# Kernel tuning notes

Hardware: AMD Instinct MI355X
Metric: run time of the kernel (lower is better)

## Reference

```python
import jax, jax.numpy as jnp
import numpy as np

E = 2048      # embed_dim
H = 16        # num_heads
HD = E // H // 2   # differential head dim = 64
S = 2048      # seq len
B = 1         # batch
DEPTH = 12
LAMBDA_INIT = 0.8 - 0.6 * float(np.exp(-0.3 * DEPTH))
EPS = 1e-5


def setup_inputs() -> dict:
    key = jax.random.key(0)
    ks = jax.random.split(key, 12)
    n = lambda k, shape, s=1.0: (jax.random.normal(k, shape, dtype=jnp.float32) * s)
    return {
        "query": n(ks[0], (S, B, E)),
        "key": n(ks[1], (S, B, E)),
        "value": n(ks[2], (S, B, E)),
        "rel_pos": 0,
        "attn_mask": jnp.zeros((B, S), dtype=jnp.bool_),
        "Wq": n(ks[3], (E, E), 0.02),
        "Wk": n(ks[4], (E, E), 0.02),
        "Wv": n(ks[5], (E, E), 0.02),
        "Wo": n(ks[6], (E, E), 0.02),
        "lq1": n(ks[7], (HD,), 0.1),
        "lk1": n(ks[8], (HD,), 0.1),
        "lq2": n(ks[9], (HD,), 0.1),
        "lk2": n(ks[10], (HD,), 0.1),
        "subln_g": jnp.ones((2 * HD,), dtype=jnp.float32),
    }


def reference(query, key, value, rel_pos, attn_mask,
              Wq, Wk, Wv, Wo, lq1, lk1, lq2, lk2, subln_g):
    # (S,B,E) -> (B,S,E)
    q = jnp.einsum("sbe,fe->bsf", query, Wq)
    k = jnp.einsum("sbe,fe->bsf", key, Wk)
    v = jnp.einsum("sbe,fe->bsf", value, Wv)

    bsz, tgt_len, _ = q.shape
    scaling = HD ** -0.5

    q = q.reshape(bsz, tgt_len, 2 * H, HD).transpose(0, 2, 1, 3) * scaling  # (B,2H,S,hd)
    k = k.reshape(bsz, tgt_len, 2 * H, HD).transpose(0, 2, 1, 3)            # (B,2H,S,hd)
    v = v.reshape(bsz, tgt_len, H, 2 * HD).transpose(0, 2, 1, 3)            # (B,H,S,2hd)

    scores = jnp.einsum("bhqd,bhkd->bhqk", q, k)  # (B,2H,S,S)
    mask = jnp.where(attn_mask[:, None, None, :], -jnp.inf, 0.0).astype(scores.dtype)
    scores = jnp.nan_to_num(scores + mask)  # torch.nan_to_num: nan->0, -inf->finite min

    probs = jax.nn.softmax(scores.astype(jnp.float32), axis=-1).astype(scores.dtype)
    probs = jnp.clip(probs, -1e6, 1e6)  # clamp as in original (dropout is identity in eval)

    lam1 = jnp.exp(jnp.sum(lq1 * lk1))
    lam2 = jnp.exp(jnp.sum(lq2 * lk2))
    lam_full = lam1 - lam2 + LAMBDA_INIT

    probs = probs.reshape(bsz, H, 2, tgt_len, tgt_len)
    diff = probs[:, :, 0] - lam_full * probs[:, :, 1]   # (B,H,S,S)

    attn = jnp.einsum("bhqk,bhkd->bhqd", diff, v)       # (B,H,S,2hd)

    # RMSNorm over last dim with affine weight
    rms = jax.lax.rsqrt(jnp.mean(jnp.square(attn), axis=-1, keepdims=True) + EPS)
    attn = attn * rms * subln_g
    attn = attn * (1.0 - LAMBDA_INIT)

    attn = attn.transpose(0, 2, 1, 3).reshape(bsz, tgt_len, H * 2 * HD)  # (B,S,E)
    attn = attn.transpose(1, 0, 2)                                       # (S,B,E)
    return jnp.einsum("sbe,fe->sbf", attn, Wo)
```

## Files before the change

kernel.cpp:

```cpp
#include <hip/hip_runtime.h>
#include <stdint.h>

#define LAMBDA_INIT_F 0.7836057665f

typedef __bf16 bf16x8 __attribute__((ext_vector_type(8)));
typedef float  f32x4  __attribute__((ext_vector_type(4)));
typedef unsigned short u16x8 __attribute__((ext_vector_type(8)));
typedef unsigned short u16x4 __attribute__((ext_vector_type(4)));
typedef short s16x4 __attribute__((ext_vector_type(4)));

__device__ __forceinline__ unsigned short f2b(float f) {
    union { float f; unsigned u; } v; v.f = f;
    unsigned u = v.u;
    return (unsigned short)((u + 0x7fffu + ((u >> 16) & 1u)) >> 16);
}

__device__ __forceinline__ unsigned pk2(float a, float b) {
    unsigned ua = __float_as_uint(a) + 0x8000u;
    unsigned ub = __float_as_uint(b) + 0x8000u;
    return __builtin_amdgcn_perm(ub, ua, 0x07060302u);
}

#if __has_builtin(__builtin_amdgcn_exp2f)
#define EXP2(x) __builtin_amdgcn_exp2f(x)
#else
__device__ __forceinline__ float EXP2(float x) {
    float r; asm volatile("v_exp_f32 %0, %1\n\ts_nop 1" : "=v"(r) : "v"(x)); return r;
}
#endif

#define GLD16(gp, sp) __builtin_amdgcn_global_load_lds( \
    (const __attribute__((address_space(1))) void*)(uintptr_t)(gp), \
    (__attribute__((address_space(3))) void*)(uint32_t)(uintptr_t)(sp), 16, 0, 0)

__global__ __launch_bounds__(256) void cvt7(const float* __restrict__ s0, const float* __restrict__ s1,
                                            const float* __restrict__ s2, const float* __restrict__ s3,
                                            const float* __restrict__ s4, const float* __restrict__ s5,
                                            const float* __restrict__ s6,
                                            unsigned short* __restrict__ dst) {
    int z = blockIdx.y;
    const float* s = z == 0 ? s0 : z == 1 ? s1 : z == 2 ? s2 : z == 3 ? s3 : z == 4 ? s4 : z == 5 ? s5 : s6;
    unsigned short* d = dst + (size_t)z * 4194304;
    size_t i = ((size_t)blockIdx.x * 256 + threadIdx.x) * 8;
    float4 a = *(const float4*)(s + i);
    float4 b = *(const float4*)(s + i + 4);
    u16x8 o;
    o[0] = f2b(a.x); o[1] = f2b(a.y); o[2] = f2b(a.z); o[3] = f2b(a.w);
    o[4] = f2b(b.x); o[5] = f2b(b.y); o[6] = f2b(b.z); o[7] = f2b(b.w);
    *(u16x8*)(d + i) = o;
}

template <int OUT_BF16, int NT, int DO_VT, int WPB>
__global__ __launch_bounds__(256, WPB) void gemm_bt(const unsigned short* __restrict__ Abase,
                                                    const unsigned short* __restrict__ Bbase,
                                                    void* __restrict__ Cbase,
                                                    unsigned short* __restrict__ VT,
                                                    float alpha0) {
    constexpr int MI = (NT == 128) ? 4 : 2;
    __shared__ __align__(16) unsigned short As[128 * 32];
    __shared__ __align__(16) unsigned short Bs[NT * 32];
    const int tid = threadIdx.x;
    const int w = tid >> 6, lane = tid & 63;
    const int quad = lane >> 4, l16 = lane & 15;
    const int b = blockIdx.z;
    const unsigned short* A = Abase + (size_t)b * 4194304;
    const unsigned short* B = Bbase + (size_t)b * 4194304;
    const float alpha = (b == 0) ? alpha0 : 1.0f;
    const int m0 = blockIdx.y * 128, n0 = blockIdx.x * NT;
    const int wm = (NT == 128) ? (w >> 1) * 64 : w * 32;
    const int wn = (NT == 128) ? (w & 1) * 64 : 0;
    const int sr = lane >> 2;
    const int sc = (((lane & 3) ^ ((lane >> 3) & 3)) * 8);
    const int rsw = ((l16 >> 1) & 3);

    f32x4 zz = {0.f, 0.f, 0.f, 0.f};
    f32x4 acc[MI][4];
#pragma unroll
    for (int i = 0; i < MI; ++i)
#pragma unroll
        for (int jn = 0; jn < 4; ++jn) acc[i][jn] = zz;

    for (int k0 = 0; k0 < 2048; k0 += 32) {
        GLD16(A + (size_t)(m0 + w * 16 + sr) * 2048 + k0 + sc,      &As[(w * 16) * 32]);
        GLD16(A + (size_t)(m0 + 64 + w * 16 + sr) * 2048 + k0 + sc, &As[(64 + w * 16) * 32]);
        if (NT == 128) {
            GLD16(B + (size_t)(n0 + w * 16 + sr) * 2048 + k0 + sc,      &Bs[(w * 16) * 32]);
            GLD16(B + (size_t)(n0 + 64 + w * 16 + sr) * 2048 + k0 + sc, &Bs[(64 + (w * 16)) * 32]);
        } else {
            GLD16(B + (size_t)(n0 + w * 16 + sr) * 2048 + k0 + sc, &Bs[(w * 16) * 32]);
        }
        __syncthreads();
        bf16x8 af[MI], bfr[4];
#pragma unroll
        for (int i = 0; i < MI; ++i) af[i]  = *(const bf16x8*)&As[(wm + i * 16 + l16) * 32 + (quad ^ rsw) * 8];
#pragma unroll
        for (int i = 0; i < 4; ++i)  bfr[i] = *(const bf16x8*)&Bs[(wn + i * 16 + l16) * 32 + (quad ^ rsw) * 8];
#pragma unroll
        for (int i = 0; i < MI; ++i)
#pragma unroll
            for (int jn = 0; jn < 4; ++jn)
                acc[i][jn] = __builtin_amdgcn_mfma_f32_16x16x32_bf16(af[i], bfr[jn], acc[i][jn], 0, 0, 0);
        __syncthreads();
    }

    if (DO_VT && b == 2) {
#pragma unroll
        for (int i = 0; i < MI; ++i)
#pragma unroll
            for (int jn = 0; jn < 4; ++jn) {
                int n = n0 + wn + jn * 16 + l16;
                int m = m0 + wm + i * 16 + quad * 4;
                u16x4 o;
#pragma unroll
                for (int r = 0; r < 4; ++r) o[r] = f2b(acc[i][jn][r]);
                *(u16x4*)&VT[(size_t)n * 2048 + m] = o;
            }
    } else {
#pragma unroll
        for (int i = 0; i < MI; ++i)
#pragma unroll
            for (int jn = 0; jn < 4; ++jn)
#pragma unroll
                for (int r = 0; r < 4; ++r) {
                    int row = m0 + wm + i * 16 + quad * 4 + r;
                    int col = n0 + wn + jn * 16 + l16;
                    float v = acc[i][jn][r] * alpha;
                    if (OUT_BF16)
                        ((unsigned short*)Cbase + (size_t)b * 4194304)[(size_t)row * 2048 + col] = f2b(v);
                    else
                        ((float*)Cbase)[(size_t)row * 2048 + col] = v;
                }
    }
}

__global__ __launch_bounds__(256, 2) void diff_attn(const unsigned short* __restrict__ qb,
                                                    const unsigned short* __restrict__ kb,
                                                    const unsigned short* __restrict__ vt,
                                                    const float* __restrict__ lq1,
                                                    const float* __restrict__ lk1,
                                                    const float* __restrict__ lq2,
                                                    const float* __restrict__ lk2,
                                                    const float* __restrict__ g,
                                                    unsigned short* __restrict__ Aout) {
    __shared__ __align__(16) unsigned short Ks[128 * 128];
    __shared__ __align__(16) unsigned short Vs[128 * 128];
    __shared__ float lam_s;
    const int tid = threadIdx.x, w = tid >> 6, lane = tid & 63;
    const int quad = lane >> 4, l16 = lane & 15;
    const int j = blockIdx.y;
    const int q0 = blockIdx.x * 64;

    if (tid < 64) {
        float p1 = lq1[tid] * lk1[tid];
        float p2 = lq2[tid] * lk2[tid];
        for (int off = 32; off; off >>= 1) { p1 += __shfl_xor(p1, off, 64); p2 += __shfl_xor(p2, off, 64); }
        if (tid == 0) lam_s = __expf(p1) - __expf(p2) + LAMBDA_INIT_F;
    }

    bf16x8 qf[2][2];
#pragma unroll
    for (int p = 0; p < 2; ++p)
#pragma unroll
        for (int dh = 0; dh < 2; ++dh)
            qf[p][dh] = *(const bf16x8*)&qb[(size_t)(q0 + w * 16 + l16) * 2048 + j * 128 + p * 64 + dh * 32 + quad * 8];

    f32x4 O[2][8];
#pragma unroll
    for (int p = 0; p < 2; ++p)
#pragma unroll
        for (int i = 0; i < 8; ++i)
#pragma unroll
            for (int r = 0; r < 4; ++r) O[p][i][r] = 0.f;
    float lsum[2] = {0.f, 0.f};

    const int srow = lane >> 4;

    for (int kv0 = 0; kv0 < 2048; kv0 += 128) {
#pragma unroll
        for (int t = 0; t < 8; ++t) {
            int rb = (w * 8 + t) * 4;
            int row = rb + srow;
            int cbs = (((lane & 15) ^ (row & 15)) * 8);
            GLD16(kb + (size_t)(kv0 + row) * 2048 + j * 128 + cbs, &Ks[rb * 128]);
            GLD16(vt + (size_t)(j * 128 + row) * 2048 + kv0 + cbs, &Vs[rb * 128]);
        }
        __syncthreads();

        s16x4 pf[2][8];
#pragma unroll
        for (int p = 0; p < 2; ++p) {
#pragma unroll
            for (int i = 0; i < 8; ++i) {
                bf16x8 a0 = *(const bf16x8*)&Ks[(i * 16 + l16) * 128 + ((p * 8 + quad) ^ l16) * 8];
                bf16x8 a1 = *(const bf16x8*)&Ks[(i * 16 + l16) * 128 + ((p * 8 + 4 + quad) ^ l16) * 8];
                f32x4 s = {0.f, 0.f, 0.f, 0.f};
                s = __builtin_amdgcn_mfma_f32_16x16x32_bf16(a0, qf[p][0], s, 0, 0, 0);
                s = __builtin_amdgcn_mfma_f32_16x16x32_bf16(a1, qf[p][1], s, 0, 0, 0);
                float e0 = EXP2(s[0]), e1 = EXP2(s[1]), e2 = EXP2(s[2]), e3 = EXP2(s[3]);
                lsum[p] += (e0 + e1) + (e2 + e3);
                unsigned d0 = pk2(e0, e1), d1 = pk2(e2, e3);
                s16x4 pv;
                pv[0] = (short)(d0 & 0xffff); pv[1] = (short)(d0 >> 16);
                pv[2] = (short)(d1 & 0xffff); pv[3] = (short)(d1 >> 16);
                pf[p][i] = pv;
            }
        }
#pragma unroll
        for (int i = 0; i < 8; ++i) {
#pragma unroll
            for (int dt = 0; dt < 8; ++dt) {
                int blk = (i * 2 + (quad >> 1)) ^ l16;
                s16x4 vf = *(const s16x4*)&Vs[(dt * 16 + l16) * 128 + blk * 8 + (quad & 1) * 4];
                O[0][dt] = __builtin_amdgcn_mfma_f32_16x16x16bf16_1k(vf, pf[0][i], O[0][dt], 0, 0, 0);
                O[1][dt] = __builtin_amdgcn_mfma_f32_16x16x16bf16_1k(vf, pf[1][i], O[1][dt], 0, 0, 0);
            }
        }
        __syncthreads();
    }

#pragma unroll
    for (int p = 0; p < 2; ++p) {
        lsum[p] += __shfl_xor(lsum[p], 16, 64);
        lsum[p] += __shfl_xor(lsum[p], 32, 64);
    }
    const float inv1 = 1.0f / lsum[0];
    const float inv2 = lam_s / lsum[1];

    float ssum = 0.f;
#pragma unroll
    for (int dt = 0; dt < 8; ++dt)
#pragma unroll
        for (int r = 0; r < 4; ++r) {
            float v = O[0][dt][r] * inv1 - O[1][dt][r] * inv2;
            O[0][dt][r] = v;
            ssum += v * v;
        }
    ssum += __shfl_xor(ssum, 16, 64);
    ssum += __shfl_xor(ssum, 32, 64);
    const float rms = rsqrtf(ssum * (1.0f / 128.0f) + 1e-5f) * (1.0f - LAMBDA_INIT_F);

#pragma unroll
    for (int dt = 0; dt < 8; ++dt) {
        float4 g4 = *(const float4*)&g[dt * 16 + quad * 4];
        u16x4 o;
        o[0] = f2b(O[0][dt][0] * rms * g4.x);
        o[1] = f2b(O[0][dt][1] * rms * g4.y);
        o[2] = f2b(O[0][dt][2] * rms * g4.z);
        o[3] = f2b(O[0][dt][3] * rms * g4.w);
        *(u16x4*)&Aout[(size_t)(q0 + w * 16 + l16) * 2048 + j * 128 + dt * 16 + quad * 4] = o;
    }
}

extern "C" void kernel_launch(void* const* d_in, const int* in_sizes, int n_in,
                              void* d_out, int out_size, void* d_ws, size_t ws_size,
                              hipStream_t stream) {
    const float* query = (const float*)d_in[0];
    const float* key   = (const float*)d_in[1];
    const float* value = (const float*)d_in[2];
    const float* Wq  = (const float*)d_in[5];
    const float* Wk  = (const float*)d_in[6];
    const float* Wv  = (const float*)d_in[7];
    const float* Wo  = (const float*)d_in[8];
    const float* lq1 = (const float*)d_in[9];
    const float* lk1 = (const float*)d_in[10];
    const float* lq2 = (const float*)d_in[11];
    const float* lk2 = (const float*)d_in[12];
    const float* g   = (const float*)d_in[13];

    char* ws = (char*)d_ws;
    const size_t MB = 1ull << 20;
    const size_t N4 = 4194304;
    unsigned short* qb  = (unsigned short*)(ws + 0 * MB);
    unsigned short* vt  = (unsigned short*)(ws + 16 * MB);
    unsigned short* Aat = (unsigned short*)(ws + 24 * MB);
    unsigned short* Xq  = (unsigned short*)(ws + 32 * MB);
    float* lamp = (float*)(ws + 96 * MB);
    (void)lamp;

    const float alpha_q = 0.125f * 1.44269504f;

    cvt7<<<dim3(2048, 7), dim3(256), 0, stream>>>(query, key, value, Wq, Wk, Wv, Wo, Xq);
    gemm_bt<1, 128, 1, 3><<<dim3(16, 16, 3), dim3(256), 0, stream>>>(Xq, Xq + 3 * N4, (void*)qb, vt, alpha_q);
    diff_attn<<<dim3(32, 16), dim3(256), 0, stream>>>(qb, qb + N4, vt, lq1, lk1, lq2, lk2, g, Aat);
    gemm_bt<0, 64, 0, 2><<<dim3(32, 16, 1), dim3(256), 0, stream>>>(Aat, Xq + 6 * N4, d_out, nullptr, 1.0f);
}
```

Baseline: 334.6 us.

## Deepen GEMM K-tile to 64, split-K output projection with atomics

Measured after the change: 352.2 us. 1.05x slower.

```diff
diff --git a/kernel.cpp b/kernel.cpp
--- a/kernel.cpp
+++ b/kernel.cpp
@@ -15,10 +15,8 @@
     return (unsigned short)((u + 0x7fffu + ((u >> 16) & 1u)) >> 16);
 }
 
-__device__ __forceinline__ unsigned pk2(float a, float b) {
-    unsigned ua = __float_as_uint(a) + 0x8000u;
-    unsigned ub = __float_as_uint(b) + 0x8000u;
-    return __builtin_amdgcn_perm(ub, ua, 0x07060302u);
+__device__ __forceinline__ unsigned pk2t(float a, float b) {
+    return __builtin_amdgcn_perm(__float_as_uint(b), __float_as_uint(a), 0x07060302u);
 }
 
 #if __has_builtin(__builtin_amdgcn_exp2f)
@@ -50,85 +48,100 @@
     *(u16x8*)(d + i) = o;
 }
 
-template <int OUT_BF16, int NT, int DO_VT, int WPB>
-__global__ __launch_bounds__(256, WPB) void gemm_bt(const unsigned short* __restrict__ Abase,
-                                                    const unsigned short* __restrict__ Bbase,
-                                                    void* __restrict__ Cbase,
-                                                    unsigned short* __restrict__ VT,
-                                                    float alpha0) {
-    constexpr int MI = (NT == 128) ? 4 : 2;
-    __shared__ __align__(16) unsigned short As[128 * 32];
-    __shared__ __align__(16) unsigned short Bs[NT * 32];
+template <int PROJ>
+__global__ __launch_bounds__(256, 2) void gemm_bt(const unsigned short* __restrict__ Abase,
+                                                  const unsigned short* __restrict__ Bbase,
+                                                  void* __restrict__ Cbase,
+                                                  unsigned short* __restrict__ VT,
+                                                  float alpha0) {
+    __shared__ __align__(16) unsigned short As[128 * 64];
+    __shared__ __align__(16) unsigned short Bs[128 * 64];
     const int tid = threadIdx.x;
     const int w = tid >> 6, lane = tid & 63;
     const int quad = lane >> 4, l16 = lane & 15;
     const int b = blockIdx.z;
-    const unsigned short* A = Abase + (size_t)b * 4194304;
-    const unsigned short* B = Bbase + (size_t)b * 4194304;
-    const float alpha = (b == 0) ? alpha0 : 1.0f;
-    const int m0 = blockIdx.y * 128, n0 = blockIdx.x * NT;
-    const int wm = (NT == 128) ? (w >> 1) * 64 : w * 32;
-    const int wn = (NT == 128) ? (w & 1) * 64 : 0;
-    const int sr = lane >> 2;
-    const int sc = (((lane & 3) ^ ((lane >> 3) & 3)) * 8);
-    const int rsw = ((l16 >> 1) & 3);
+    const unsigned short* A = PROJ ? Abase + (size_t)b * 4194304 : Abase;
+    const unsigned short* B = PROJ ? Bbase + (size_t)b * 4194304 : Bbase;
+    const int kbeg = PROJ ? 0 : b * 1024;
+    const int kend = PROJ ? 2048 : (b * 1024 + 1024);
+    const float alpha = (PROJ && b != 0) ? 1.0f : alpha0;
+    const int m0 = blockIdx.y * 128, n0 = blockIdx.x * 128;
+    const int wm = (w >> 1) * 64, wn = (w & 1) * 64;
+    const int sr8 = lane >> 3;
+    const int sblk = lane & 7;
+    const int rk = l16 & 7;
 
     f32x4 zz = {0.f, 0.f, 0.f, 0.f};
-    f32x4 acc[MI][4];
-#pragma unroll
-    for (int i = 0; i < MI; ++i)
+    f32x4 acc[4][4];
+#pragma unroll
+    for (int i = 0; i < 4; ++i)
 #pragma unroll
         for (int jn = 0; jn < 4; ++jn) acc[i][jn] = zz;
 
-    for (int k0 = 0; k0 < 2048; k0 += 32) {
-        GLD16(A + (size_t)(m0 + w * 16 + sr) * 2048 + k0 + sc,      &As[(w * 16) * 32]);
-        GLD16(A + (size_t)(m0 + 64 + w * 16 + sr) * 2048 + k0 + sc, &As[(64 + w * 16) * 32]);
-        if (NT == 128) {
-            GLD16(B + (size_t)(n0 + w * 16 + sr) * 2048 + k0 + sc,      &Bs[(w * 16) * 32]);
-            GLD16(B + (size_t)(n0 + 64 + w * 16 + sr) * 2048 + k0 + sc, &Bs[(64 + (w * 16)) * 32]);
+    for (int k0 = kbeg; k0 < kend; k0 += 64) {
+#pragma unroll
+        for (int t = 0; t < 4; ++t) {
+            int rb = w * 32 + t * 8;
+            int ra = rb + sr8;
+            int ca = (sblk ^ (ra & 7)) * 8;
+            GLD16(A + (size_t)(m0 + ra) * 2048 + k0 + ca, &As[rb * 64]);
+            GLD16(B + (size_t)(n0 + ra) * 2048 + k0 + ca, &Bs[rb * 64]);
+        }
+        __syncthreads();
+#pragma unroll
+        for (int ks = 0; ks < 2; ++ks) {
+            bf16x8 af[4], bfr[4];
+#pragma unroll
+            for (int i = 0; i < 4; ++i)
+                af[i]  = *(const bf16x8*)&As[(wm + i * 16 + l16) * 64 + ((ks * 4 + quad) ^ rk) * 8];
+#pragma unroll
+            for (int i = 0; i < 4; ++i)
+                bfr[i] = *(const bf16x8*)&Bs[(wn + i * 16 + l16) * 64 + ((ks * 4 + quad) ^ rk) * 8];
+#pragma unroll
+            for (int i = 0; i < 4; ++i)
+#pragma unroll
+                for (int jn = 0; jn < 4; ++jn)
+                    acc[i][jn] = __builtin_amdgcn_mfma_f32_16x16x32_bf16(af[i], bfr[jn], acc[i][jn], 0, 0, 0);
+        }
+        __syncthreads();
+    }
+
+    if (PROJ) {
+        if (b == 2) {
+#pragma unroll
+            for (int i = 0; i < 4; ++i)
+#pragma unroll
+                for (int jn = 0; jn < 4; ++jn) {
+                    int n = n0 + wn + jn * 16 + l16;
+                    int m = m0 + wm + i * 16 + quad * 4;
+                    u16x4 o;
+#pragma unroll
+                    for (int r = 0; r < 4; ++r) o[r] = f2b(acc[i][jn][r]);
+                    *(u16x4*)&VT[(size_t)n * 2048 + m] = o;
+                }
         } else {
-            GLD16(B + (size_t)(n0 + w * 16 + sr) * 2048 + k0 + sc, &Bs[(w * 16) * 32]);
-        }
-        __syncthreads();
-        bf16x8 af[MI], bfr[4];
-#pragma unroll
-        for (int i = 0; i < MI; ++i) af[i]  = *(const bf16x8*)&As[(wm + i * 16 + l16) * 32 + (quad ^ rsw) * 8];
-#pragma unroll
-        for (int i = 0; i < 4; ++i)  bfr[i] = *(const bf16x8*)&Bs[(wn + i * 16 + l16) * 32 + (quad ^ rsw) * 8];
-#pragma unroll
-        for (int i = 0; i < MI; ++i)
-#pragma unroll
-            for (int jn = 0; jn < 4; ++jn)
-                acc[i][jn] = __builtin_amdgcn_mfma_f32_16x16x32_bf16(af[i], bfr[jn], acc[i][jn], 0, 0, 0);
-        __syncthreads();
-    }
-
-    if (DO_VT && b == 2) {
-#pragma unroll
-        for (int i = 0; i < MI; ++i)
-#pragma unroll
-            for (int jn = 0; jn < 4; ++jn) {
-                int n = n0 + wn + jn * 16 + l16;
-                int m = m0 + wm + i * 16 + quad * 4;
-                u16x4 o;
-#pragma unroll
-                for (int r = 0; r < 4; ++r) o[r] = f2b(acc[i][jn][r]);
-                *(u16x4*)&VT[(size_t)n * 2048 + m] = o;
-            }
+#pragma unroll
+            for (int i = 0; i < 4; ++i)
+#pragma unroll
+                for (int jn = 0; jn < 4; ++jn)
+#pragma unroll
+                    for (int r = 0; r < 4; ++r) {
+                        int row = m0 + wm + i * 16 + quad * 4 + r;
+                        int col = n0 + wn + jn * 16 + l16;
+                        ((unsigned short*)Cbase + (size_t)b * 4194304)[(size_t)row * 2048 + col] =
+                            f2b(acc[i][jn][r] * alpha);
+                    }
+        }
     } else {
 #pragma unroll
-        for (int i = 0; i < MI; ++i)
+        for (int i = 0; i < 4; ++i)
 #pragma unroll
             for (int jn = 0; jn < 4; ++jn)
 #pragma unroll
                 for (int r = 0; r < 4; ++r) {
                     int row = m0 + wm + i * 16 + quad * 4 + r;
                     int col = n0 + wn + jn * 16 + l16;
-                    float v = acc[i][jn][r] * alpha;
-                    if (OUT_BF16)
-                        ((unsigned short*)Cbase + (size_t)b * 4194304)[(size_t)row * 2048 + col] = f2b(v);
-                    else
-                        ((float*)Cbase)[(size_t)row * 2048 + col] = v;
+                    atomicAdd(&((float*)Cbase)[(size_t)row * 2048 + col], acc[i][jn][r]);
                 }
     }
 }
@@ -198,7 +211,7 @@
                 s = __builtin_amdgcn_mfma_f32_16x16x32_bf16(a1, qf[p][1], s, 0, 0, 0);
                 float e0 = EXP2(s[0]), e1 = EXP2(s[1]), e2 = EXP2(s[2]), e3 = EXP2(s[3]);
                 lsum[p] += (e0 + e1) + (e2 + e3);
-                unsigned d0 = pk2(e0, e1), d1 = pk2(e2, e3);
+                unsigned d0 = pk2t(e0, e1), d1 = pk2t(e2, e3);
                 s16x4 pv;
                 pv[0] = (short)(d0 & 0xffff); pv[1] = (short)(d0 >> 16);
                 pv[2] = (short)(d1 & 0xffff); pv[3] = (short)(d1 >> 16);
@@ -274,13 +287,12 @@
     unsigned short* vt  = (unsigned short*)(ws + 16 * MB);
     unsigned short* Aat = (unsigned short*)(ws + 24 * MB);
     unsigned short* Xq  = (unsigned short*)(ws + 32 * MB);
-    float* lamp = (float*)(ws + 96 * MB);
-    (void)lamp;
 
     const float alpha_q = 0.125f * 1.44269504f;
 
     cvt7<<<dim3(2048, 7), dim3(256), 0, stream>>>(query, key, value, Wq, Wk, Wv, Wo, Xq);
-    gemm_bt<1, 128, 1, 3><<<dim3(16, 16, 3), dim3(256), 0, stream>>>(Xq, Xq + 3 * N4, (void*)qb, vt, alpha_q);
+    gemm_bt<1><<<dim3(16, 16, 3), dim3(256), 0, stream>>>(Xq, Xq + 3 * N4, (void*)qb, vt, alpha_q);
     diff_attn<<<dim3(32, 16), dim3(256), 0, stream>>>(qb, qb + N4, vt, lq1, lk1, lq2, lk2, g, Aat);
-    gemm_bt<0, 64, 0, 2><<<dim3(32, 16, 1), dim3(256), 0, stream>>>(Aat, Xq + 6 * N4, d_out, nullptr, 1.0f);
-}
+    hipMemsetAsync(d_out, 0, (size_t)out_size * sizeof(float), stream);
+    gemm_bt<0><<<dim3(16, 16, 2), dim3(256), 0, stream>>>(Aat, Xq + 6 * N4, d_out, nullptr, 1.0f);
+}
```
